# Optimization experiments

Measured on AMD Instinct MI355X. Metric: run time of the kernel, lower is better.

The kernel has to match this reference:

```python
import jax, jax.numpy as jnp
import numpy as np

B, S, T, D, V = 512, 128, 128, 512, 128  # batch, enc len, dec steps (=longest_smi), dim_model, output_size


def setup_inputs() -> dict:
    key = jax.random.key(0)
    ks = jax.random.split(key, 17)
    sc = 0.05
    return {
        "e_all": jax.random.normal(ks[0], (B, S, D), jnp.float32),
        "e_h": jax.random.normal(ks[1], (1, B, D), jnp.float32),
        "e_c": jax.random.normal(ks[2], (1, B, D), jnp.float32),
        "target": jax.random.randint(ks[3], (B, T), 0, T),
        # params (Linear weights stored [in, out], y = x @ W + b)
        "E": jax.random.normal(ks[4], (T, D), jnp.float32) * sc,        # Embedding(longest_smi, D)
        "Wa": jax.random.normal(ks[5], (D, D), jnp.float32) * sc,
        "ba": jnp.zeros((D,), jnp.float32),
        "Ua": jax.random.normal(ks[6], (D, D), jnp.float32) * sc,
        "bu": jnp.zeros((D,), jnp.float32),
        "Va": jax.random.normal(ks[7], (D, 1), jnp.float32) * sc,
        "bv": jnp.zeros((1,), jnp.float32),
        "W_ih": jax.random.normal(ks[8], (2 * D, 4 * D), jnp.float32) * sc,
        "b_ih": jnp.zeros((4 * D,), jnp.float32),
        "W_hh": jax.random.normal(ks[9], (D, 4 * D), jnp.float32) * sc,
        "b_hh": jnp.zeros((4 * D,), jnp.float32),
        "W_out": jax.random.normal(ks[10], (D, V), jnp.float32) * sc,
        "b_out": jnp.zeros((V,), jnp.float32),
    }


def reference(e_all, e_h, e_c, target, E, Wa, ba, Ua, bu, Va, bv,
              W_ih, b_ih, W_hh, b_hh, W_out, b_out):
    Bb = e_all.shape[0]
    # teacher forcing: step 0 input is token 0 (SOS), then target[:, :-1]
    idx = jnp.concatenate([jnp.zeros((Bb, 1), target.dtype), target[:, :-1]], axis=1)  # [B,T]
    emb_all = E[idx]                       # [B,T,D] (dropout is identity in eval)
    keys_proj = e_all @ Ua + bu            # Ua(keys), loop-invariant  [B,S,D]
    h0, c0 = e_h[0], e_c[0]                # [B,D]

    def step(carry, emb):
        h, c = carry
        q = (h + c) @ Wa + ba                                   # [B,D]  Wa(query)
        s = jnp.tanh(q[:, None, :] + keys_proj) @ Va + bv       # [B,S,1]
        w = jax.nn.softmax(s[..., 0], axis=-1)                  # [B,S]
        ctx = jnp.einsum('bs,bsd->bd', w, e_all)                # [B,D]
        x = jnp.concatenate([emb, ctx], axis=-1)                # [B,2D]
        g = x @ W_ih + b_ih + h @ W_hh + b_hh                   # [B,4D], torch gate order i,f,g,o
        i_, f_, g_, o_ = jnp.split(g, 4, axis=-1)
        c2 = jax.nn.sigmoid(f_) * c + jax.nn.sigmoid(i_) * jnp.tanh(g_)
        h2 = jax.nn.sigmoid(o_) * jnp.tanh(c2)
        out = h2 @ W_out + b_out                                # [B,V]
        return (h2, c2), (out, w)

    _, (outs, attns) = jax.lax.scan(step, (h0, c0), jnp.swapaxes(emb_all, 0, 1))
    outputs = jax.nn.log_softmax(jnp.swapaxes(outs, 0, 1), axis=-1)  # [B,T,V]
    cross_attn = jnp.swapaxes(attns, 0, 1)                           # [B,T,S]
    return outputs, cross_attn
```

## Files before the change

### kernel.cpp

```cpp
#include <hip/hip_runtime.h>

#define B_ 512
#define S_ 128
#define T_ 128
#define D_ 512
#define V_ 128
#define LDW 72

typedef __attribute__((ext_vector_type(8))) short s16x8;
typedef __attribute__((ext_vector_type(4))) short s16x4;
typedef __attribute__((ext_vector_type(4))) float f32x4;

__device__ __forceinline__ float b2f(unsigned short h) {
    union { unsigned int u; float f; } x; x.u = ((unsigned int)h) << 16; return x.f;
}
__device__ __forceinline__ unsigned short f2b(float f) {
    union { float f; unsigned int u; } x; x.f = f;
    unsigned int u = x.u; u += 0x7FFFu + ((u >> 16) & 1u);
    return (unsigned short)(u >> 16);
}
#if __has_builtin(__builtin_amdgcn_rcpf)
__device__ __forceinline__ float rcp_f(float x) { return __builtin_amdgcn_rcpf(x); }
#else
__device__ __forceinline__ float rcp_f(float x) { return 1.0f / x; }
#endif
__device__ __forceinline__ float sigm(float x) { return rcp_f(1.0f + __expf(-x)); }
__device__ __forceinline__ float tanh_fast(float x) {
    float e = __expf(2.0f * fabsf(x));
    float r = 1.0f - 2.0f * rcp_f(e + 1.0f);
    return copysignf(r, x);
}
__device__ __forceinline__ float tanh_pade(float x) {
    float t = x * x;
    float num = x * fmaf(t, 105.0f + t, 945.0f);
    float den = fmaf(t, fmaf(t, 15.0f, 420.0f), 945.0f);
    float r = num * rcp_f(den);
    return fminf(1.0f, fmaxf(-1.0f, r));
}

#if __has_builtin(__builtin_amdgcn_cvt_f32_fp8)
__device__ __forceinline__ f32x4 fp8x4_dec(unsigned w) {
    f32x4 r;
    r[0] = __builtin_amdgcn_cvt_f32_fp8(w, 0);
    r[1] = __builtin_amdgcn_cvt_f32_fp8(w, 1);
    r[2] = __builtin_amdgcn_cvt_f32_fp8(w, 2);
    r[3] = __builtin_amdgcn_cvt_f32_fp8(w, 3);
    return r;
}
#else
__device__ __forceinline__ float fp8_dec_sw(unsigned w, int j) {
    unsigned char v = (w >> (8 * j)) & 0xFF;
    unsigned s = v >> 7, e = (v >> 3) & 0xF, m = v & 7;
    float r = (e == 0) ? ldexpf((float)m, -9) : ldexpf((float)(8 + m), (int)e - 10);
    return s ? -r : r;
}
__device__ __forceinline__ f32x4 fp8x4_dec(unsigned w) {
    f32x4 r;
    r[0] = fp8_dec_sw(w, 0); r[1] = fp8_dec_sw(w, 1);
    r[2] = fp8_dec_sw(w, 2); r[3] = fp8_dec_sw(w, 3);
    return r;
}
#endif

#if __has_builtin(__builtin_amdgcn_cvt_pk_fp8_f32)
__device__ __forceinline__ unsigned pk_fp8(float a, float b, float c, float d) {
    int r = 0;
    r = __builtin_amdgcn_cvt_pk_fp8_f32(a, b, r, false);
    r = __builtin_amdgcn_cvt_pk_fp8_f32(c, d, r, true);
    return (unsigned)r;
}
#else
__device__ __forceinline__ unsigned char f32_to_fp8_sw(float x) {
    unsigned s = x < 0.f ? 0x80u : 0u; float a = fabsf(x);
    if (a != a) return (unsigned char)(s | 0x7F);
    if (a >= 448.f) return (unsigned char)(s | 0x7E);
    if (a < 0.001953125f) { int m = (int)rintf(a * 512.0f); return (unsigned char)(s | (m > 7 ? 0x08 : m)); }
    int e; float fr = frexpf(a, &e);
    int m = (int)rintf(fr * 16.0f - 8.0f);
    int ee = e - 1 + 7;
    if (m == 8) { m = 0; ee += 1; }
    if (ee <= 0) { int mm = (int)rintf(a * 512.f); return (unsigned char)(s | (mm > 7 ? 0x08 : mm)); }
    if (ee >= 16) return (unsigned char)(s | 0x7E);
    return (unsigned char)(s | (ee << 3) | m);
}
__device__ __forceinline__ unsigned pk_fp8(float a, float b, float c, float d) {
    return (unsigned)f32_to_fp8_sw(a) | ((unsigned)f32_to_fp8_sw(b) << 8)
         | ((unsigned)f32_to_fp8_sw(c) << 16) | ((unsigned)f32_to_fp8_sw(d) << 24);
}
#endif

struct P {
    const int* target;
    const float* E; const float* bv; const float* ba; const float* bout;
    const short* vab;
    const unsigned char* ea8; const unsigned char* kp8;
    const short* WaT; const short* WehT; const short* WctxT; const short* WoutT;
    const float* bcat;
    short* qbf; short* xeh; short* ctxb; short* gpA; short* gpB;
    short* hcbf; short* h2bf; float* cst;
    float* out_logits; float* out_attn;
};

struct AttnS { float scp[4][64]; float wbuf[S_]; float cpart[4][D_]; };
struct OutS  { short As[64][LDW]; short Bs[128][LDW]; };
struct PG2   { short As[128][LDW]; short Bs[64][LDW]; };
struct GateS { short As[64][LDW]; short Bs[64][LDW]; float gt[64][65]; };
union SharedC { OutS o; PG2 g; };

__device__ __forceinline__ void attn_phase(const P& p, AttnS& sh, int b, int step)
{
    const int t = threadIdx.x, lane = t & 63, wave = t >> 6;
    {
        const int sg = wave & 1, dh = wave >> 1;
        const int s = sg * 64 + lane;
        const unsigned char* kb = p.kp8 + (size_t)b * (S_ * D_);
        const short* qv = p.qbf + (size_t)b * D_;
        float acc = 0.f;
        #pragma unroll 4
        for (int i = 0; i < 16; ++i) {
            int g = dh * 16 + i;
            uint4 kw = *(const uint4*)(kb + ((size_t)g * 128 + s) * 16);
            const short* qg = qv + g * 16;
            const short* vg = p.vab + g * 16;
            s16x8 q0 = *(const s16x8*)(qg), q1 = *(const s16x8*)(qg + 8);
            s16x8 v0 = *(const s16x8*)(vg), v1 = *(const s16x8*)(vg + 8);
            f32x4 ka = fp8x4_dec(kw.x), kb4 = fp8x4_dec(kw.y);
            f32x4 kc = fp8x4_dec(kw.z), kd = fp8x4_dec(kw.w);
            #pragma unroll
            for (int j = 0; j < 4; ++j) {
                acc += tanh_pade(b2f((unsigned short)q0[j])     + ka[j])  * b2f((unsigned short)v0[j]);
                acc += tanh_pade(b2f((unsigned short)q0[4 + j]) + kb4[j]) * b2f((unsigned short)v0[4 + j]);
                acc += tanh_pade(b2f((unsigned short)q1[j])     + kc[j])  * b2f((unsigned short)v1[j]);
                acc += tanh_pade(b2f((unsigned short)q1[4 + j]) + kd[j])  * b2f((unsigned short)v1[4 + j]);
            }
        }
        sh.scp[wave][lane] = acc;
    }
    __syncthreads();
    if (wave == 0) {
        const float bvv = p.bv[0];
        float v0 = sh.scp[0][lane] + sh.scp[2][lane] + bvv;
        float v1 = sh.scp[1][lane] + sh.scp[3][lane] + bvv;
        float m = fmaxf(v0, v1);
        #pragma unroll
        for (int o = 32; o >= 1; o >>= 1) m = fmaxf(m, __shfl_xor(m, o));
        float e0 = __expf(v0 - m), e1 = __expf(v1 - m);
        float su = e0 + e1;
        #pragma unroll
        for (int o = 32; o >= 1; o >>= 1) su += __shfl_xor(su, o);
        float inv = rcp_f(su);
        float w0 = e0 * inv, w1 = e1 * inv;
        sh.wbuf[lane] = w0; sh.wbuf[lane + 64] = w1;
        float* ao = p.out_attn + ((size_t)b * T_ + step) * S_;
        ao[lane] = w0; ao[lane + 64] = w1;
    }
    __syncthreads();
    {
        const int d0 = lane * 8;
        f32x4 aA = {0.f,0.f,0.f,0.f}, aB = {0.f,0.f,0.f,0.f};
        const unsigned char* eb = p.ea8 + (size_t)b * S_ * D_ + d0;
        #pragma unroll 4
        for (int i = 0; i < 32; ++i) {
            int s = wave * 32 + i;
            float wv = sh.wbuf[s];
            uint2 ev = *(const uint2*)(eb + (size_t)s * D_);
            f32x4 ex = fp8x4_dec(ev.x), ey = fp8x4_dec(ev.y);
            #pragma unroll
            for (int j = 0; j < 4; ++j) aA[j] += wv * ex[j];
            #pragma unroll
            for (int j = 0; j < 4; ++j) aB[j] += wv * ey[j];
        }
        *(f32x4*)&sh.cpart[wave][d0]     = aA;
        *(f32x4*)&sh.cpart[wave][d0 + 4] = aB;
    }
    __syncthreads();
    {
        int dd = t * 2;
        float v0 = sh.cpart[0][dd]   + sh.cpart[1][dd]   + sh.cpart[2][dd]   + sh.cpart[3][dd];
        float v1 = sh.cpart[0][dd+1] + sh.cpart[1][dd+1] + sh.cpart[2][dd+1] + sh.cpart[3][dd+1];
        short2 o2; o2.x = (short)f2b(v0); o2.y = (short)f2b(v1);
        *(short2*)(p.ctxb + (size_t)b * D_ + dd) = o2;
    }
}

__device__ __forceinline__ void pgate_phase(const P& p, PG2& sh, int bid2, int koff,
                                            short* __restrict__ gpp, bool addb)
{
    const int t = threadIdx.x, lane = t & 63, wave = t >> 6;
    const int lrow = lane & 15, kq = lane >> 4;
    const int m0 = (bid2 >> 5) * 128, n0 = (bid2 & 31) * 64;
    f32x4 acc[2][4] = {};
    for (int k0 = 0; k0 < 512; k0 += 64) {
        s16x8 va[4], vb[2];
        #pragma unroll
        for (int r = 0; r < 4; ++r) {
            int idx = r * 256 + t, row = idx >> 3, seg = idx & 7;
            va[r] = *(const s16x8*)(p.xeh + (size_t)(m0 + row) * 1024 + koff + k0 + seg * 8);
        }
        #pragma unroll
        for (int r = 0; r < 2; ++r) {
            int idx = r * 256 + t, row = idx >> 3, seg = idx & 7;
            vb[r] = *(const s16x8*)(p.WehT + (size_t)(n0 + row) * 1024 + koff + k0 + seg * 8);
        }
        __syncthreads();
        #pragma unroll
        for (int r = 0; r < 4; ++r) {
            int idx = r * 256 + t, row = idx >> 3, seg = idx & 7;
            *(s16x8*)(&sh.As[row][seg * 8]) = va[r];
        }
        #pragma unroll
        for (int r = 0; r < 2; ++r) {
            int idx = r * 256 + t, row = idx >> 3, seg = idx & 7;
            *(s16x8*)(&sh.Bs[row][seg * 8]) = vb[r];
        }
        __syncthreads();
        #pragma unroll
        for (int kk = 0; kk < 64; kk += 32) {
            s16x8 af[2], bf[4];
            af[0] = *(const s16x8*)(&sh.As[wave * 32 + lrow][kk + kq * 8]);
            af[1] = *(const s16x8*)(&sh.As[wave * 32 + 16 + lrow][kk + kq * 8]);
            #pragma unroll
            for (int f = 0; f < 4; ++f)
                bf[f] = *(const s16x8*)(&sh.Bs[f * 16 + lrow][kk + kq * 8]);
            #pragma unroll
            for (int m2 = 0; m2 < 2; ++m2)
                #pragma unroll
                for (int n2 = 0; n2 < 4; ++n2)
                    acc[m2][n2] = __builtin_amdgcn_mfma_f32_16x16x32_bf16(af[m2], bf[n2], acc[m2][n2], 0, 0, 0);
        }
    }
    #pragma unroll
    for (int m2 = 0; m2 < 2; ++m2)
        #pragma unroll
        for (int n2 = 0; n2 < 4; ++n2) {
            int col = n0 + n2 * 16 + lrow;
            float bvv = addb ? p.bcat[col] : 0.0f;
            #pragma unroll
            for (int j = 0; j < 4; ++j) {
                int row = m0 + wave * 32 + m2 * 16 + kq * 4 + j;
                gpp[(size_t)row * 2048 + col] = (short)f2b(acc[m2][n2][j] + bvv);
            }
        }
}

__device__ __forceinline__ void fgate_phase(const P& p, GateS& sh, int bid, int step)
{
    const int t = threadIdx.x, lane = t & 63, wave = t >> 6;
    const int wr = wave >> 1, wc = wave & 1;
    const int lrow = lane & 15, kq = lane >> 4;
    const int srow = t >> 3, sseg = t & 7;
    const int m0 = (bid >> 5) * 64, n0 = (bid & 31) * 64;
    f32x4 acc[2][2] = {};
    for (int k0 = 0; k0 < 512; k0 += 64) {
        s16x8 va0 = *(const s16x8*)(p.ctxb + (size_t)(m0 + srow) * 512 + k0 + sseg * 8);
        s16x8 va1 = *(const s16x8*)(p.ctxb + (size_t)(m0 + srow + 32) * 512 + k0 + sseg * 8);
        s16x8 vb0 = *(const s16x8*)(p.WctxT + (size_t)(n0 + srow) * 512 + k0 + sseg * 8);
        s16x8 vb1 = *(const s16x8*)(p.WctxT + (size_t)(n0 + srow + 32) * 512 + k0 + sseg * 8);
        __syncthreads();
        *(s16x8*)(&sh.As[srow][sseg * 8]) = va0;
        *(s16x8*)(&sh.As[srow + 32][sseg * 8]) = va1;
        *(s16x8*)(&sh.Bs[srow][sseg * 8]) = vb0;
        *(s16x8*)(&sh.Bs[srow + 32][sseg * 8]) = vb1;
        __syncthreads();
        #pragma unroll
        for (int kk = 0; kk < 64; kk += 32) {
            s16x8 af0 = *(const s16x8*)(&sh.As[wr * 32 + lrow][kk + kq * 8]);
            s16x8 af1 = *(const s16x8*)(&sh.As[wr * 32 + 16 + lrow][kk + kq * 8]);
            s16x8 bf0 = *(const s16x8*)(&sh.Bs[wc * 32 + lrow][kk + kq * 8]);
            s16x8 bf1 = *(const s16x8*)(&sh.Bs[wc * 32 + 16 + lrow][kk + kq * 8]);
            acc[0][0] = __builtin_amdgcn_mfma_f32_16x16x32_bf16(af0, bf0, acc[0][0], 0, 0, 0);
            acc[0][1] = __builtin_amdgcn_mfma_f32_16x16x32_bf16(af0, bf1, acc[0][1], 0, 0, 0);
            acc[1][0] = __builtin_amdgcn_mfma_f32_16x16x32_bf16(af1, bf0, acc[1][0], 0, 0, 0);
            acc[1][1] = __builtin_amdgcn_mfma_f32_16x16x32_bf16(af1, bf1, acc[1][1], 0, 0, 0);
        }
    }
    #pragma unroll
    for (int m2 = 0; m2 < 2; ++m2)
        #pragma unroll
        for (int n2 = 0; n2 < 2; ++n2) {
            int cl = wc * 32 + n2 * 16 + lrow;
            #pragma unroll
            for (int j = 0; j < 4; ++j) {
                int rl = wr * 32 + m2 * 16 + kq * 4 + j;
                size_t gidx = (size_t)(m0 + rl) * 2048 + n0 + cl;
                sh.gt[rl][cl] = acc[m2][n2][j]
                              + b2f((unsigned short)p.gpA[gidx])
                              + b2f((unsigned short)p.gpB[gidx]);
            }
        }
    __syncthreads();
    const int rl4 = t >> 4, dl = t & 15;
    #pragma unroll
    for (int pass = 0; pass < 4; ++pass) {
        int row = pass * 16 + rl4;
        int b = m0 + row;
        int d = (n0 >> 2) + dl;
        float gi = sh.gt[row][dl * 4 + 0];
        float gf = sh.gt[row][dl * 4 + 1];
        float gg = sh.gt[row][dl * 4 + 2];
        float go = sh.gt[row][dl * 4 + 3];
        float cv = p.cst[(size_t)b * D_ + d];
        float c2 = sigm(gf) * cv + sigm(gi) * tanh_fast(gg);
        float h2 = sigm(go) * tanh_fast(c2);
        p.cst[(size_t)b * D_ + d] = c2;
        p.hcbf[(size_t)b * D_ + d] = (short)f2b(h2 + c2);
        p.h2bf[(size_t)b * D_ + d] = (short)f2b(h2);
        p.xeh[(size_t)b * 1024 + 512 + d] = (short)f2b(h2);
        int tok = p.target[b * T_ + step];
        p.xeh[(size_t)b * 1024 + d] = (short)f2b(p.E[(size_t)tok * D_ + d]);
    }
}

__device__ __forceinline__ void q_phase(const P& p, OutS& sh, int bid)
{
    const int t = threadIdx.x, lane = t & 63, wave = t >> 6;
    const int lrow = lane & 15, kq = lane >> 4;
    const int srow = t >> 3, sseg = t & 7;
    const int m0 = (bid >> 4) * 64, n0 = (bid & 15) * 32;
    f32x4 acc0 = {}, acc1 = {};
    for (int k0 = 0; k0 < 512; k0 += 64) {
        s16x8 va0 = *(const s16x8*)(p.hcbf + (size_t)(m0 + srow) * 512 + k0 + sseg * 8);
        s16x8 va1 = *(const s16x8*)(p.hcbf + (size_t)(m0 + srow + 32) * 512 + k0 + sseg * 8);
        int brow = n0 + (srow & 31);
        s16x8 vb0 = *(const s16x8*)(p.WaT + (size_t)brow * 512 + k0 + sseg * 8);
        __syncthreads();
        *(s16x8*)(&sh.As[srow][sseg * 8]) = va0;
        *(s16x8*)(&sh.As[srow + 32][sseg * 8]) = va1;
        if (srow < 32) *(s16x8*)(&sh.Bs[srow][sseg * 8]) = vb0;
        __syncthreads();
        #pragma unroll
        for (int kk = 0; kk < 64; kk += 32) {
            s16x8 af  = *(const s16x8*)(&sh.As[wave * 16 + lrow][kk + kq * 8]);
            s16x8 bf0 = *(const s16x8*)(&sh.Bs[lrow][kk + kq * 8]);
            s16x8 bf1 = *(const s16x8*)(&sh.Bs[16 + lrow][kk + kq * 8]);
            acc0 = __builtin_amdgcn_mfma_f32_16x16x32_bf16(af, bf0, acc0, 0, 0, 0);
            acc1 = __builtin_amdgcn_mfma_f32_16x16x32_bf16(af, bf1, acc1, 0, 0, 0);
        }
    }
    #pragma unroll
    for (int n2 = 0; n2 < 2; ++n2) {
        int col = n0 + n2 * 16 + lrow;
        float bvv = p.ba[col];
        f32x4 av = n2 ? acc1 : acc0;
        #pragma unroll
        for (int j = 0; j < 4; ++j) {
            int row = m0 + wave * 16 + kq * 4 + j;
            p.qbf[(size_t)row * 512 + col] = (short)f2b(av[j] + bvv);
        }
    }
}

__device__ __forceinline__ void out_phase(const P& p, OutS& sh, int obid, int step)
{
    const int t = threadIdx.x, lane = t & 63, wave = t >> 6;
    const int lrow = lane & 15, kq = lane >> 4;
    const int srow = t >> 3, sseg = t & 7;
    const int m0 = obid * 64;
    f32x4 acc[8] = {};
    for (int k0 = 0; k0 < 512; k0 += 64) {
        s16x8 va0 = *(const s16x8*)(p.h2bf + (size_t)(m0 + srow) * 512 + k0 + sseg * 8);
        s16x8 va1 = *(const s16x8*)(p.h2bf + (size_t)(m0 + srow + 32) * 512 + k0 + sseg * 8);
        s16x8 vb[4];
        #pragma unroll
        for (int p4 = 0; p4 < 4; ++p4)
            vb[p4] = *(const s16x8*)(p.WoutT + (size_t)(srow + p4 * 32) * 512 + k0 + sseg * 8);
        __syncthreads();
        *(s16x8*)(&sh.As[srow][sseg * 8]) = va0;
        *(s16x8*)(&sh.As[srow + 32][sseg * 8]) = va1;
        #pragma unroll
        for (int p4 = 0; p4 < 4; ++p4) *(s16x8*)(&sh.Bs[srow + p4 * 32][sseg * 8]) = vb[p4];
        __syncthreads();
        #pragma unroll
        for (int kk = 0; kk < 64; kk += 32) {
            s16x8 a = *(const s16x8*)(&sh.As[wave * 16 + lrow][kk + kq * 8]);
            #pragma unroll
            for (int f = 0; f < 8; ++f) {
                s16x8 b = *(const s16x8*)(&sh.Bs[f * 16 + lrow][kk + kq * 8]);
                acc[f] = __builtin_amdgcn_mfma_f32_16x16x32_bf16(a, b, acc[f], 0, 0, 0);
            }
        }
    }
    float colb[8];
    #pragma unroll
    for (int f = 0; f < 8; ++f) colb[f] = p.bout[f * 16 + lrow];
    #pragma unroll
    for (int j = 0; j < 4; ++j) {
        float v[8]; float mx = -1e30f;
        #pragma unroll
        for (int f = 0; f < 8; ++f) { v[f] = acc[f][j] + colb[f]; mx = fmaxf(mx, v[f]); }
        #pragma unroll
        for (int o = 1; o < 16; o <<= 1) mx = fmaxf(mx, __shfl_xor(mx, o));
        float sum = 0.f;
        #pragma unroll
        for (int f = 0; f < 8; ++f) sum += __expf(v[f] - mx);
        #pragma unroll
        for (int o = 1; o < 16; o <<= 1) sum += __shfl_xor(sum, o);
        float lse = mx + __logf(sum);
        int row = m0 + wave * 16 + kq * 4 + j;
        float* orow = p.out_logits + ((size_t)row * T_ + step) * V_;
        #pragma unroll
        for (int f = 0; f < 8; ++f) orow[f * 16 + lrow] = v[f] - lse;
    }
}

__global__ __launch_bounds__(256, 2) void kA(P p, int step) {
    __shared__ AttnS sh;
    attn_phase(p, sh, blockIdx.x, step);
}
__global__ __launch_bounds__(256, 2) void kB(P p, int step) {
    __shared__ GateS sh;
    fgate_phase(p, sh, blockIdx.x, step);
}
template<bool INIT>
__global__ __launch_bounds__(256, 2) void kC(P p, int step) {
    __shared__ SharedC sh;
    const int bid = blockIdx.x;
    if (bid < 128)       q_phase(p, sh.o, bid);
    else if (bid < 256)  pgate_phase(p, sh.g, bid - 128, 0,   p.gpA, true);
    else if (bid < 384)  pgate_phase(p, sh.g, bid - 256, 512, p.gpB, false);
    else if (!INIT)      out_phase(p, sh.o, bid - 384, step);
}

__global__ __launch_bounds__(256)
void gemm64(const short* __restrict__ A, const short* __restrict__ Bt,
            const float* __restrict__ bias, short* __restrict__ Cp,
            int M, int N, int K)
{
    __shared__ __align__(16) short As[64][LDW];
    __shared__ __align__(16) short Bs[64][LDW];
    const int t = threadIdx.x;
    const int lane = t & 63, wave = t >> 6;
    const int wr = wave >> 1, wc = wave & 1;
    const int lrow = lane & 15, kq = lane >> 4;
    const int m0 = blockIdx.y * 64, n0 = blockIdx.x * 64;
    const int srow = t >> 3, sseg = t & 7;
    f32x4 acc[2][2] = {};
    for (int k0 = 0; k0 < K; k0 += 64) {
        s16x8 va0 = *(const s16x8*)(A + (size_t)(m0 + srow) * K + k0 + sseg * 8);
        s16x8 va1 = *(const s16x8*)(A + (size_t)(m0 + srow + 32) * K + k0 + sseg * 8);
        s16x8 vb0 = *(const s16x8*)(Bt + (size_t)(n0 + srow) * K + k0 + sseg * 8);
        s16x8 vb1 = *(const s16x8*)(Bt + (size_t)(n0 + srow + 32) * K + k0 + sseg * 8);
        __syncthreads();
        *(s16x8*)(&As[srow][sseg * 8]) = va0;
        *(s16x8*)(&As[srow + 32][sseg * 8]) = va1;
        *(s16x8*)(&Bs[srow][sseg * 8]) = vb0;
        *(s16x8*)(&Bs[srow + 32][sseg * 8]) = vb1;
        __syncthreads();
        for (int kk = 0; kk < 64; kk += 32) {
            s16x8 af[2], bf[2];
            af[0] = *(const s16x8*)(&As[wr * 32 + lrow][kk + kq * 8]);
            af[1] = *(const s16x8*)(&As[wr * 32 + 16 + lrow][kk + kq * 8]);
            bf[0] = *(const s16x8*)(&Bs[wc * 32 + lrow][kk + kq * 8]);
            bf[1] = *(const s16x8*)(&Bs[wc * 32 + 16 + lrow][kk + kq * 8]);
            for (int m2 = 0; m2 < 2; ++m2)
                for (int n2 = 0; n2 < 2; ++n2)
                    acc[m2][n2] = __builtin_amdgcn_mfma_f32_16x16x32_bf16(af[m2], bf[n2], acc[m2][n2], 0, 0, 0);
        }
    }
    for (int m2 = 0; m2 < 2; ++m2)
        for (int n2 = 0; n2 < 2; ++n2) {
            int col = n0 + wc * 32 + n2 * 16 + lrow;
            float bvv = bias ? bias[col] : 0.0f;
            for (int j = 0; j < 4; ++j) {
                int row = m0 + wr * 32 + m2 * 16 + kq * 4 + j;
                Cp[(size_t)row * N + col] = (short)f2b(acc[m2][n2][j] + bvv);
            }
        }
}

__global__ __launch_bounds__(256)
void transpose_kp8(const short* __restrict__ in, unsigned char* __restrict__ out)
{
    const int b = blockIdx.x, t = threadIdx.x;
    const size_t ibase = (size_t)b * (S_ * D_);
    for (int k = t; k < 32 * S_; k += 256) {
        int g = k >> 7, s = k & 127;
        const short* src = in + ibase + (size_t)s * D_ + g * 16;
        unsigned w[4];
        #pragma unroll
        for (int q4 = 0; q4 < 4; ++q4) {
            w[q4] = pk_fp8(b2f((unsigned short)src[q4 * 4 + 0]), b2f((unsigned short)src[q4 * 4 + 1]),
                           b2f((unsigned short)src[q4 * 4 + 2]), b2f((unsigned short)src[q4 * 4 + 3]));
        }
        uint4 o; o.x = w[0]; o.y = w[1]; o.z = w[2]; o.w = w[3];
        *(uint4*)(out + ibase + ((size_t)g * S_ + s) * 16) = o;
    }
}

__global__ __launch_bounds__(256)
void cast_fp8_v4(const float* __restrict__ in, unsigned char* __restrict__ out, int n4)
{
    int i = blockIdx.x * 256 + threadIdx.x;
    int stride = gridDim.x * 256;
    for (; i < n4; i += stride) {
        f32x4 v = ((const f32x4*)in)[i];
        ((unsigned*)out)[i] = pk_fp8(v[0], v[1], v[2], v[3]);
    }
}

__global__ __launch_bounds__(256)
void init_state(const float* __restrict__ e_h, const float* __restrict__ e_c,
                float* __restrict__ c, short* __restrict__ hcbf,
                short* __restrict__ xeh, const float* __restrict__ E)
{
    int gid = blockIdx.x * 256 + threadIdx.x;
    int b = gid >> 9, d = gid & 511;
    float h0 = e_h[gid], c0 = e_c[gid];
    c[gid] = c0;
    hcbf[gid] = (short)f2b(h0 + c0);
    xeh[(size_t)b * 1024 + 512 + d] = (short)f2b(h0);
    xeh[(size_t)b * 1024 + d] = (short)f2b(E[d]);
}

__global__ __launch_bounds__(256)
void transpose_cast(const float* __restrict__ in, short* __restrict__ out,
                    int N, int ostride, int koff, int gate_perm)
{
    __shared__ float tile[64][65];
    int t = threadIdx.x;
    int n0 = blockIdx.x * 64, k0 = blockIdx.y * 64;
    int cc = t & 63, r4 = t >> 6;
    for (int i = 0; i < 16; ++i) {
        int r = i * 4 + r4;
        tile[r][cc] = in[(size_t)(k0 + r) * N + n0 + cc];
    }
    __syncthreads();
    for (int i = 0; i < 16; ++i) {
        int nr = i * 4 + r4;
        int ng = n0 + nr;
        int np = gate_perm ? ((ng & 511) * 4 + (ng >> 9)) : ng;
        out[(size_t)np * ostride + koff + k0 + cc] = (short)f2b(tile[cc][nr]);
    }
}

__global__ __launch_bounds__(256)
void cast_bf16_v4(const float* __restrict__ in, short* __restrict__ out, int n4)
{
    int i = blockIdx.x * 256 + threadIdx.x;
    int stride = gridDim.x * 256;
    for (; i < n4; i += stride) {
        f32x4 v = ((const f32x4*)in)[i];
        s16x4 o;
        for (int j = 0; j < 4; ++j) o[j] = (short)f2b(v[j]);
        ((s16x4*)out)[i] = o;
    }
}

__global__ __launch_bounds__(256)
void make_bcat(const float* __restrict__ b_ih, const float* __restrict__ b_hh, float* __restrict__ bcat)
{
    int i = blockIdx.x * 256 + threadIdx.x;
    if (i < 2048) {
        int np = (i & 511) * 4 + (i >> 9);
        bcat[np] = b_ih[i] + b_hh[i];
    }
}

extern "C" void kernel_launch(void* const* d_in, const int* in_sizes, int n_in,
                              void* d_out, int out_size, void* d_ws, size_t ws_size,
                              hipStream_t stream)
{
    const float* e_all  = (const float*)d_in[0];
    const float* e_h    = (const float*)d_in[1];
    const float* e_c    = (const float*)d_in[2];
    const int*   target = (const int*)d_in[3];
    const float* E      = (const float*)d_in[4];
    const float* Wa     = (const float*)d_in[5];
    const float* ba     = (const float*)d_in[6];
    const float* Ua     = (const float*)d_in[7];
    const float* bu     = (const float*)d_in[8];
    const float* Va     = (const float*)d_in[9];
    const float* bv     = (const float*)d_in[10];
    const float* W_ih   = (const float*)d_in[11];
    const float* b_ih   = (const float*)d_in[12];
    const float* W_hh   = (const float*)d_in[13];
    const float* b_hh   = (const float*)d_in[14];
    const float* W_out  = (const float*)d_in[15];
    const float* b_out  = (const float*)d_in[16];

    char* ws = (char*)d_ws;
    size_t off = 0;
    auto alloc = [&](size_t bytes) { void* p = ws + off; off += (bytes + 255) & ~255ull; return p; };
    short* ealb  = (short*)alloc((size_t)B_ * S_ * D_ * 2);
    short* kpb   = (short*)alloc((size_t)B_ * S_ * D_ * 2);
    unsigned char* kp8 = (unsigned char*)alloc((size_t)B_ * S_ * D_);
    unsigned char* ea8 = (unsigned char*)alloc((size_t)B_ * S_ * D_);
    short* WaT   = (short*)alloc((size_t)D_ * D_ * 2);
    short* UaT   = (short*)alloc((size_t)D_ * D_ * 2);
    short* WehT  = (short*)alloc((size_t)2048 * 1024 * 2);
    short* WctxT = (short*)alloc((size_t)2048 * 512 * 2);
    short* WoutT = (short*)alloc((size_t)V_ * D_ * 2);
    float* bcat  = (float*)alloc(2048 * 4);
    short* qbf   = (short*)alloc((size_t)B_ * D_ * 2);
    short* vab   = (short*)alloc((size_t)D_ * 2);
    short* xeh   = (short*)alloc((size_t)B_ * 1024 * 2);
    short* ctxb  = (short*)alloc((size_t)B_ * D_ * 2);
    short* gpA   = (short*)alloc((size_t)B_ * 2048 * 2);
    short* gpB   = (short*)alloc((size_t)B_ * 2048 * 2);
    short* hcbf  = (short*)alloc((size_t)B_ * D_ * 2);
    short* h2bf  = (short*)alloc((size_t)B_ * D_ * 2);
    float* cst   = (float*)alloc((size_t)B_ * D_ * 4);
    if (off > ws_size) return;

    float* out_logits = (float*)d_out;
    float* out_attn   = (float*)d_out + (size_t)B_ * T_ * V_;

    cast_bf16_v4<<<4096, 256, 0, stream>>>(e_all, ealb, B_ * S_ * D_ / 4);
    cast_fp8_v4<<<4096, 256, 0, stream>>>(e_all, ea8, B_ * S_ * D_ / 4);
    cast_bf16_v4<<<1,    256, 0, stream>>>(Va, vab, D_ / 4);
    transpose_cast<<<dim3(8, 8),  256, 0, stream>>>(Wa,  WaT,  512,  512, 0, 0);
    transpose_cast<<<dim3(8, 8),  256, 0, stream>>>(Ua,  UaT,  512,  512, 0, 0);
    transpose_cast<<<dim3(32, 8), 256, 0, stream>>>(W_ih,              WehT,  2048, 1024, 0,   1);
    transpose_cast<<<dim3(32, 8), 256, 0, stream>>>(W_ih + 512 * 2048, WctxT, 2048, 512,  0,   1);
    transpose_cast<<<dim3(32, 8), 256, 0, stream>>>(W_hh,              WehT,  2048, 1024, 512, 1);
    transpose_cast<<<dim3(2, 8),  256, 0, stream>>>(W_out, WoutT, 128, 512, 0, 0);
    make_bcat<<<8, 256, 0, stream>>>(b_ih, b_hh, bcat);
    gemm64<<<dim3(8, 1024), 256, 0, stream>>>(ealb, UaT, bu, kpb, B_ * S_, 512, 512);
    transpose_kp8<<<512, 256, 0, stream>>>(kpb, kp8);
    init_state<<<1024, 256, 0, stream>>>(e_h, e_c, cst, hcbf, xeh, E);

    P pp;
    pp.target = target; pp.E = E; pp.bv = bv; pp.ba = ba; pp.bout = b_out;
    pp.vab = vab;
    pp.ea8 = ea8; pp.kp8 = kp8; pp.WaT = WaT; pp.WehT = WehT; pp.WctxT = WctxT; pp.WoutT = WoutT;
    pp.bcat = bcat; pp.qbf = qbf; pp.xeh = xeh; pp.ctxb = ctxb; pp.gpA = gpA; pp.gpB = gpB;
    pp.hcbf = hcbf; pp.h2bf = h2bf; pp.cst = cst;
    pp.out_logits = out_logits; pp.out_attn = out_attn;

    kC<true><<<384, 256, 0, stream>>>(pp, 0);

    for (int t = 0; t < T_; ++t) {
        kA<<<512, 256, 0, stream>>>(pp, t);
        kB<<<256, 256, 0, stream>>>(pp, t);
        kC<false><<<392, 256, 0, stream>>>(pp, t);
    }
    (void)n_in; (void)in_sizes; (void)out_size;
}
```

Before: 6.259 ms.

## Fuse query projection into attention and merge per-step kernels into two launches

Removes the separate q=(h+c)@Wa GEMM by computing it inside the attention block, with each block handling two batch rows. The attention kernel now also runs the full-K emb/h gate pre-GEMM (the two half-K partials are merged into one buffer) and the previous step's output projection, so each time step needs two launches instead of three. The aim is to cut launch and inter-kernel sync overhead and the extra global round trips for q and the partial gates. In exchange, the q projection runs on scalar FMAs that re-read Wa for every pair of rows, and attention blocks do more serial work each.

```diff
diff --git a/kernel.cpp b/kernel.cpp
--- a/kernel.cpp
+++ b/kernel.cpp
@@ -91,36 +91,67 @@
 
 struct P {
     const int* target;
-    const float* E; const float* bv; const float* ba; const float* bout;
+    const float* E; const float* bv; const float* ba; const float* bout; const float* bcat;
     const short* vab;
     const unsigned char* ea8; const unsigned char* kp8;
-    const short* WaT; const short* WehT; const short* WctxT; const short* WoutT;
-    const float* bcat;
-    short* qbf; short* xeh; short* ctxb; short* gpA; short* gpB;
-    short* hcbf; short* h2bf; float* cst;
+    const short* Wab; const short* WehT; const short* WctxT; const short* WoutT;
+    short* ctxb; short* gp;
+    float* cst; short* hcbf; short* h2bf; short* xeh;
     float* out_logits; float* out_attn;
 };
 
-struct AttnS { float scp[4][64]; float wbuf[S_]; float cpart[4][D_]; };
+struct Attn2S {
+    float hcl[2][512];
+    float part[4][512];
+    short qbls[2][512];
+    float scp[4][64];
+    float wbuf[2][128];
+};
+struct PG2   { short As[128][LDW]; short Bs[64][LDW]; };
 struct OutS  { short As[64][LDW]; short Bs[128][LDW]; };
-struct PG2   { short As[128][LDW]; short Bs[64][LDW]; };
 struct GateS { short As[64][LDW]; short Bs[64][LDW]; float gt[64][65]; };
-union SharedC { OutS o; PG2 g; };
-
-__device__ __forceinline__ void attn_phase(const P& p, AttnS& sh, int b, int step)
+union SharedD1 { Attn2S a; PG2 pg; OutS o; };
+
+__device__ __forceinline__ void attn2_phase(const P& p, Attn2S& sh, int pairIdx, int step)
 {
     const int t = threadIdx.x, lane = t & 63, wave = t >> 6;
+    const int r = wave >> 1;
+    const int b0 = pairIdx * 2;
+    for (int i = t; i < 1024; i += 256) {
+        int rr = i >> 9, d = i & 511;
+        sh.hcl[rr][d] = b2f((unsigned short)p.hcbf[(size_t)(b0 + rr) * 512 + d]);
+    }
+    __syncthreads();
     {
-        const int sg = wave & 1, dh = wave >> 1;
+        const int kh = wave & 1;
+        const short* wb = p.Wab + (size_t)(kh * 256) * 512 + lane * 8;
+        float qa[8] = {};
+        #pragma unroll 4
+        for (int k = 0; k < 256; ++k) {
+            s16x8 wv = *(const s16x8*)(wb + (size_t)k * 512);
+            float h = sh.hcl[r][kh * 256 + k];
+            #pragma unroll
+            for (int j = 0; j < 8; ++j) qa[j] += h * b2f((unsigned short)wv[j]);
+        }
+        #pragma unroll
+        for (int j = 0; j < 8; ++j) sh.part[wave][lane * 8 + j] = qa[j];
+    }
+    __syncthreads();
+    for (int i = t; i < 1024; i += 256) {
+        int rr = i >> 9, c = i & 511;
+        float qv = sh.part[rr * 2][c] + sh.part[rr * 2 + 1][c] + p.ba[c];
+        sh.qbls[rr][c] = (short)f2b(qv);
+    }
+    __syncthreads();
+    {
+        const int sg = wave & 1;
         const int s = sg * 64 + lane;
-        const unsigned char* kb = p.kp8 + (size_t)b * (S_ * D_);
-        const short* qv = p.qbf + (size_t)b * D_;
+        const unsigned char* kb = p.kp8 + (size_t)(b0 + r) * (S_ * D_);
         float acc = 0.f;
-        #pragma unroll 4
-        for (int i = 0; i < 16; ++i) {
-            int g = dh * 16 + i;
+        #pragma unroll 2
+        for (int g = 0; g < 32; ++g) {
             uint4 kw = *(const uint4*)(kb + ((size_t)g * 128 + s) * 16);
-            const short* qg = qv + g * 16;
+            const short* qg = &sh.qbls[r][g * 16];
             const short* vg = p.vab + g * 16;
             s16x8 q0 = *(const s16x8*)(qg), q1 = *(const s16x8*)(qg + 8);
             s16x8 v0 = *(const s16x8*)(vg), v1 = *(const s16x8*)(vg + 8);
@@ -137,10 +168,10 @@
         sh.scp[wave][lane] = acc;
     }
     __syncthreads();
-    if (wave == 0) {
+    if ((wave & 1) == 0) {
         const float bvv = p.bv[0];
-        float v0 = sh.scp[0][lane] + sh.scp[2][lane] + bvv;
-        float v1 = sh.scp[1][lane] + sh.scp[3][lane] + bvv;
+        float v0 = sh.scp[wave][lane] + bvv;
+        float v1 = sh.scp[wave + 1][lane] + bvv;
         float m = fmaxf(v0, v1);
         #pragma unroll
         for (int o = 32; o >= 1; o >>= 1) m = fmaxf(m, __shfl_xor(m, o));
@@ -150,19 +181,20 @@
         for (int o = 32; o >= 1; o >>= 1) su += __shfl_xor(su, o);
         float inv = rcp_f(su);
         float w0 = e0 * inv, w1 = e1 * inv;
-        sh.wbuf[lane] = w0; sh.wbuf[lane + 64] = w1;
-        float* ao = p.out_attn + ((size_t)b * T_ + step) * S_;
+        sh.wbuf[r][lane] = w0; sh.wbuf[r][lane + 64] = w1;
+        float* ao = p.out_attn + ((size_t)(b0 + r) * T_ + step) * S_;
         ao[lane] = w0; ao[lane + 64] = w1;
     }
     __syncthreads();
     {
+        const int sg = wave & 1;
         const int d0 = lane * 8;
         f32x4 aA = {0.f,0.f,0.f,0.f}, aB = {0.f,0.f,0.f,0.f};
-        const unsigned char* eb = p.ea8 + (size_t)b * S_ * D_ + d0;
+        const unsigned char* eb = p.ea8 + (size_t)(b0 + r) * S_ * D_ + d0;
         #pragma unroll 4
-        for (int i = 0; i < 32; ++i) {
-            int s = wave * 32 + i;
-            float wv = sh.wbuf[s];
+        for (int i = 0; i < 64; ++i) {
+            int s = sg * 64 + i;
+            float wv = sh.wbuf[r][s];
             uint2 ev = *(const uint2*)(eb + (size_t)s * D_);
             f32x4 ex = fp8x4_dec(ev.x), ey = fp8x4_dec(ev.y);
             #pragma unroll
@@ -170,37 +202,39 @@
             #pragma unroll
             for (int j = 0; j < 4; ++j) aB[j] += wv * ey[j];
         }
-        *(f32x4*)&sh.cpart[wave][d0]     = aA;
-        *(f32x4*)&sh.cpart[wave][d0 + 4] = aB;
+        *(f32x4*)&sh.part[wave][d0]     = aA;
+        *(f32x4*)&sh.part[wave][d0 + 4] = aB;
     }
     __syncthreads();
     {
         int dd = t * 2;
-        float v0 = sh.cpart[0][dd]   + sh.cpart[1][dd]   + sh.cpart[2][dd]   + sh.cpart[3][dd];
-        float v1 = sh.cpart[0][dd+1] + sh.cpart[1][dd+1] + sh.cpart[2][dd+1] + sh.cpart[3][dd+1];
-        short2 o2; o2.x = (short)f2b(v0); o2.y = (short)f2b(v1);
-        *(short2*)(p.ctxb + (size_t)b * D_ + dd) = o2;
-    }
-}
-
-__device__ __forceinline__ void pgate_phase(const P& p, PG2& sh, int bid2, int koff,
-                                            short* __restrict__ gpp, bool addb)
+        #pragma unroll
+        for (int rr = 0; rr < 2; ++rr) {
+            float v0 = sh.part[rr * 2][dd]     + sh.part[rr * 2 + 1][dd];
+            float v1 = sh.part[rr * 2][dd + 1] + sh.part[rr * 2 + 1][dd + 1];
+            short2 o2; o2.x = (short)f2b(v0); o2.y = (short)f2b(v1);
+            *(short2*)(p.ctxb + (size_t)(b0 + rr) * D_ + dd) = o2;
+        }
+    }
+}
+
+__device__ __forceinline__ void pgate_full(const P& p, PG2& sh, int bid2)
 {
     const int t = threadIdx.x, lane = t & 63, wave = t >> 6;
     const int lrow = lane & 15, kq = lane >> 4;
     const int m0 = (bid2 >> 5) * 128, n0 = (bid2 & 31) * 64;
     f32x4 acc[2][4] = {};
-    for (int k0 = 0; k0 < 512; k0 += 64) {
+    for (int k0 = 0; k0 < 1024; k0 += 64) {
         s16x8 va[4], vb[2];
         #pragma unroll
         for (int r = 0; r < 4; ++r) {
             int idx = r * 256 + t, row = idx >> 3, seg = idx & 7;
-            va[r] = *(const s16x8*)(p.xeh + (size_t)(m0 + row) * 1024 + koff + k0 + seg * 8);
+            va[r] = *(const s16x8*)(p.xeh + (size_t)(m0 + row) * 1024 + k0 + seg * 8);
         }
         #pragma unroll
         for (int r = 0; r < 2; ++r) {
             int idx = r * 256 + t, row = idx >> 3, seg = idx & 7;
-            vb[r] = *(const s16x8*)(p.WehT + (size_t)(n0 + row) * 1024 + koff + k0 + seg * 8);
+            vb[r] = *(const s16x8*)(p.WehT + (size_t)(n0 + row) * 1024 + k0 + seg * 8);
         }
         __syncthreads();
         #pragma unroll
@@ -234,21 +268,76 @@
         #pragma unroll
         for (int n2 = 0; n2 < 4; ++n2) {
             int col = n0 + n2 * 16 + lrow;
-            float bvv = addb ? p.bcat[col] : 0.0f;
+            float bvv = p.bcat[col];
             #pragma unroll
             for (int j = 0; j < 4; ++j) {
                 int row = m0 + wave * 32 + m2 * 16 + kq * 4 + j;
-                gpp[(size_t)row * 2048 + col] = (short)f2b(acc[m2][n2][j] + bvv);
+                p.gp[(size_t)row * 2048 + col] = (short)f2b(acc[m2][n2][j] + bvv);
             }
         }
 }
 
-__device__ __forceinline__ void fgate_phase(const P& p, GateS& sh, int bid, int step)
-{
+__device__ __forceinline__ void out_phase(const P& p, OutS& sh, int obid, int step)
+{
+    const int t = threadIdx.x, lane = t & 63, wave = t >> 6;
+    const int lrow = lane & 15, kq = lane >> 4;
+    const int srow = t >> 3, sseg = t & 7;
+    const int m0 = obid * 64;
+    f32x4 acc[8] = {};
+    for (int k0 = 0; k0 < 512; k0 += 64) {
+        s16x8 va0 = *(const s16x8*)(p.h2bf + (size_t)(m0 + srow) * 512 + k0 + sseg * 8);
+        s16x8 va1 = *(const s16x8*)(p.h2bf + (size_t)(m0 + srow + 32) * 512 + k0 + sseg * 8);
+        s16x8 vb[4];
+        #pragma unroll
+        for (int p4 = 0; p4 < 4; ++p4)
+            vb[p4] = *(const s16x8*)(p.WoutT + (size_t)(srow + p4 * 32) * 512 + k0 + sseg * 8);
+        __syncthreads();
+        *(s16x8*)(&sh.As[srow][sseg * 8]) = va0;
+        *(s16x8*)(&sh.As[srow + 32][sseg * 8]) = va1;
+        #pragma unroll
+        for (int p4 = 0; p4 < 4; ++p4) *(s16x8*)(&sh.Bs[srow + p4 * 32][sseg * 8]) = vb[p4];
+        __syncthreads();
+        #pragma unroll
+        for (int kk = 0; kk < 64; kk += 32) {
+            s16x8 a = *(const s16x8*)(&sh.As[wave * 16 + lrow][kk + kq * 8]);
+            #pragma unroll
+            for (int f = 0; f < 8; ++f) {
+                s16x8 b = *(const s16x8*)(&sh.Bs[f * 16 + lrow][kk + kq * 8]);
+                acc[f] = __builtin_amdgcn_mfma_f32_16x16x32_bf16(a, b, acc[f], 0, 0, 0);
+            }
+        }
+    }
+    float colb[8];
+    #pragma unroll
+    for (int f = 0; f < 8; ++f) colb[f] = p.bout[f * 16 + lrow];
+    #pragma unroll
+    for (int j = 0; j < 4; ++j) {
+        float v[8]; float mx = -1e30f;
+        #pragma unroll
+        for (int f = 0; f < 8; ++f) { v[f] = acc[f][j] + colb[f]; mx = fmaxf(mx, v[f]); }
+        #pragma unroll
+        for (int o = 1; o < 16; o <<= 1) mx = fmaxf(mx, __shfl_xor(mx, o));
+        float sum = 0.f;
+        #pragma unroll
+        for (int f = 0; f < 8; ++f) sum += __expf(v[f] - mx);
+        #pragma unroll
+        for (int o = 1; o < 16; o <<= 1) sum += __shfl_xor(sum, o);
+        float lse = mx + __logf(sum);
+        int row = m0 + wave * 16 + kq * 4 + j;
+        float* orow = p.out_logits + ((size_t)row * T_ + step) * V_;
+        #pragma unroll
+        for (int f = 0; f < 8; ++f) orow[f * 16 + lrow] = v[f] - lse;
+    }
+}
+
+__global__ __launch_bounds__(256, 2) void kB(P p, int step)
+{
+    __shared__ GateS sh;
     const int t = threadIdx.x, lane = t & 63, wave = t >> 6;
     const int wr = wave >> 1, wc = wave & 1;
     const int lrow = lane & 15, kq = lane >> 4;
     const int srow = t >> 3, sseg = t & 7;
+    const int bid = blockIdx.x;
     const int m0 = (bid >> 5) * 64, n0 = (bid & 31) * 64;
     f32x4 acc[2][2] = {};
     for (int k0 = 0; k0 < 512; k0 += 64) {
@@ -282,143 +371,54 @@
             #pragma unroll
             for (int j = 0; j < 4; ++j) {
                 int rl = wr * 32 + m2 * 16 + kq * 4 + j;
-                size_t gidx = (size_t)(m0 + rl) * 2048 + n0 + cl;
                 sh.gt[rl][cl] = acc[m2][n2][j]
-                              + b2f((unsigned short)p.gpA[gidx])
-                              + b2f((unsigned short)p.gpB[gidx]);
+                              + b2f((unsigned short)p.gp[(size_t)(m0 + rl) * 2048 + n0 + cl]);
             }
         }
     __syncthreads();
-    const int rl4 = t >> 4, dl = t & 15;
+    const int dp = t & 7, rr = t >> 3;
     #pragma unroll
-    for (int pass = 0; pass < 4; ++pass) {
-        int row = pass * 16 + rl4;
+    for (int pass = 0; pass < 2; ++pass) {
+        int row = pass * 32 + rr;
         int b = m0 + row;
-        int d = (n0 >> 2) + dl;
-        float gi = sh.gt[row][dl * 4 + 0];
-        float gf = sh.gt[row][dl * 4 + 1];
-        float gg = sh.gt[row][dl * 4 + 2];
-        float go = sh.gt[row][dl * 4 + 3];
-        float cv = p.cst[(size_t)b * D_ + d];
-        float c2 = sigm(gf) * cv + sigm(gi) * tanh_fast(gg);
-        float h2 = sigm(go) * tanh_fast(c2);
-        p.cst[(size_t)b * D_ + d] = c2;
-        p.hcbf[(size_t)b * D_ + d] = (short)f2b(h2 + c2);
-        p.h2bf[(size_t)b * D_ + d] = (short)f2b(h2);
-        p.xeh[(size_t)b * 1024 + 512 + d] = (short)f2b(h2);
+        int dl0 = dp * 2;
+        float gi0 = sh.gt[row][dl0 * 4 + 0], gf0 = sh.gt[row][dl0 * 4 + 1];
+        float gg0 = sh.gt[row][dl0 * 4 + 2], go0 = sh.gt[row][dl0 * 4 + 3];
+        float gi1 = sh.gt[row][dl0 * 4 + 4], gf1 = sh.gt[row][dl0 * 4 + 5];
+        float gg1 = sh.gt[row][dl0 * 4 + 6], go1 = sh.gt[row][dl0 * 4 + 7];
+        int d = (n0 >> 2) + dl0;
+        float2 cv = *(const float2*)(p.cst + (size_t)b * 512 + d);
+        float c20 = sigm(gf0) * cv.x + sigm(gi0) * tanh_fast(gg0);
+        float h20 = sigm(go0) * tanh_fast(c20);
+        float c21 = sigm(gf1) * cv.y + sigm(gi1) * tanh_fast(gg1);
+        float h21 = sigm(go1) * tanh_fast(c21);
+        float2 cw; cw.x = c20; cw.y = c21;
+        *(float2*)(p.cst + (size_t)b * 512 + d) = cw;
+        unsigned hcp = (unsigned)f2b(h20 + c20) | ((unsigned)f2b(h21 + c21) << 16);
+        unsigned h2p = (unsigned)f2b(h20) | ((unsigned)f2b(h21) << 16);
+        *(unsigned*)(p.hcbf + (size_t)b * 512 + d) = hcp;
+        *(unsigned*)(p.h2bf + (size_t)b * 512 + d) = h2p;
+        *(unsigned*)(p.xeh + (size_t)b * 1024 + 512 + d) = h2p;
         int tok = p.target[b * T_ + step];
-        p.xeh[(size_t)b * 1024 + d] = (short)f2b(p.E[(size_t)tok * D_ + d]);
-    }
-}
-
-__device__ __forceinline__ void q_phase(const P& p, OutS& sh, int bid)
-{
-    const int t = threadIdx.x, lane = t & 63, wave = t >> 6;
-    const int lrow = lane & 15, kq = lane >> 4;
-    const int srow = t >> 3, sseg = t & 7;
-    const int m0 = (bid >> 4) * 64, n0 = (bid & 15) * 32;
-    f32x4 acc0 = {}, acc1 = {};
-    for (int k0 = 0; k0 < 512; k0 += 64) {
-        s16x8 va0 = *(const s16x8*)(p.hcbf + (size_t)(m0 + srow) * 512 + k0 + sseg * 8);
-        s16x8 va1 = *(const s16x8*)(p.hcbf + (size_t)(m0 + srow + 32) * 512 + k0 + sseg * 8);
-        int brow = n0 + (srow & 31);
-        s16x8 vb0 = *(const s16x8*)(p.WaT + (size_t)brow * 512 + k0 + sseg * 8);
-        __syncthreads();
-        *(s16x8*)(&sh.As[srow][sseg * 8]) = va0;
-        *(s16x8*)(&sh.As[srow + 32][sseg * 8]) = va1;
-        if (srow < 32) *(s16x8*)(&sh.Bs[srow][sseg * 8]) = vb0;
-        __syncthreads();
-        #pragma unroll
-        for (int kk = 0; kk < 64; kk += 32) {
-            s16x8 af  = *(const s16x8*)(&sh.As[wave * 16 + lrow][kk + kq * 8]);
-            s16x8 bf0 = *(const s16x8*)(&sh.Bs[lrow][kk + kq * 8]);
-            s16x8 bf1 = *(const s16x8*)(&sh.Bs[16 + lrow][kk + kq * 8]);
-            acc0 = __builtin_amdgcn_mfma_f32_16x16x32_bf16(af, bf0, acc0, 0, 0, 0);
-            acc1 = __builtin_amdgcn_mfma_f32_16x16x32_bf16(af, bf1, acc1, 0, 0, 0);
-        }
-    }
-    #pragma unroll
-    for (int n2 = 0; n2 < 2; ++n2) {
-        int col = n0 + n2 * 16 + lrow;
-        float bvv = p.ba[col];
-        f32x4 av = n2 ? acc1 : acc0;
-        #pragma unroll
-        for (int j = 0; j < 4; ++j) {
-            int row = m0 + wave * 16 + kq * 4 + j;
-            p.qbf[(size_t)row * 512 + col] = (short)f2b(av[j] + bvv);
-        }
-    }
-}
-
-__device__ __forceinline__ void out_phase(const P& p, OutS& sh, int obid, int step)
-{
-    const int t = threadIdx.x, lane = t & 63, wave = t >> 6;
-    const int lrow = lane & 15, kq = lane >> 4;
-    const int srow = t >> 3, sseg = t & 7;
-    const int m0 = obid * 64;
-    f32x4 acc[8] = {};
-    for (int k0 = 0; k0 < 512; k0 += 64) {
-        s16x8 va0 = *(const s16x8*)(p.h2bf + (size_t)(m0 + srow) * 512 + k0 + sseg * 8);
-        s16x8 va1 = *(const s16x8*)(p.h2bf + (size_t)(m0 + srow + 32) * 512 + k0 + sseg * 8);
-        s16x8 vb[4];
-        #pragma unroll
-        for (int p4 = 0; p4 < 4; ++p4)
-            vb[p4] = *(const s16x8*)(p.WoutT + (size_t)(srow + p4 * 32) * 512 + k0 + sseg * 8);
-        __syncthreads();
-        *(s16x8*)(&sh.As[srow][sseg * 8]) = va0;
-        *(s16x8*)(&sh.As[srow + 32][sseg * 8]) = va1;
-        #pragma unroll
-        for (int p4 = 0; p4 < 4; ++p4) *(s16x8*)(&sh.Bs[srow + p4 * 32][sseg * 8]) = vb[p4];
-        __syncthreads();
-        #pragma unroll
-        for (int kk = 0; kk < 64; kk += 32) {
-            s16x8 a = *(const s16x8*)(&sh.As[wave * 16 + lrow][kk + kq * 8]);
-            #pragma unroll
-            for (int f = 0; f < 8; ++f) {
-                s16x8 b = *(const s16x8*)(&sh.Bs[f * 16 + lrow][kk + kq * 8]);
-                acc[f] = __builtin_amdgcn_mfma_f32_16x16x32_bf16(a, b, acc[f], 0, 0, 0);
-            }
-        }
-    }
-    float colb[8];
-    #pragma unroll
-    for (int f = 0; f < 8; ++f) colb[f] = p.bout[f * 16 + lrow];
-    #pragma unroll
-    for (int j = 0; j < 4; ++j) {
-        float v[8]; float mx = -1e30f;
-        #pragma unroll
-        for (int f = 0; f < 8; ++f) { v[f] = acc[f][j] + colb[f]; mx = fmaxf(mx, v[f]); }
-        #pragma unroll
-        for (int o = 1; o < 16; o <<= 1) mx = fmaxf(mx, __shfl_xor(mx, o));
-        float sum = 0.f;
-        #pragma unroll
-        for (int f = 0; f < 8; ++f) sum += __expf(v[f] - mx);
-        #pragma unroll
-        for (int o = 1; o < 16; o <<= 1) sum += __shfl_xor(sum, o);
-        float lse = mx + __logf(sum);
-        int row = m0 + wave * 16 + kq * 4 + j;
-        float* orow = p.out_logits + ((size_t)row * T_ + step) * V_;
-        #pragma unroll
-        for (int f = 0; f < 8; ++f) orow[f * 16 + lrow] = v[f] - lse;
-    }
-}
-
-__global__ __launch_bounds__(256, 2) void kA(P p, int step) {
-    __shared__ AttnS sh;
-    attn_phase(p, sh, blockIdx.x, step);
-}
-__global__ __launch_bounds__(256, 2) void kB(P p, int step) {
-    __shared__ GateS sh;
-    fgate_phase(p, sh, blockIdx.x, step);
-}
-template<bool INIT>
-__global__ __launch_bounds__(256, 2) void kC(P p, int step) {
-    __shared__ SharedC sh;
+        unsigned ep = (unsigned)f2b(p.E[(size_t)tok * 512 + d])
+                    | ((unsigned)f2b(p.E[(size_t)tok * 512 + d + 1]) << 16);
+        *(unsigned*)(p.xeh + (size_t)b * 1024 + d) = ep;
+    }
+}
+
+__global__ __launch_bounds__(256, 2) void kD1(P p, int step)
+{
+    __shared__ SharedD1 sh;
     const int bid = blockIdx.x;
-    if (bid < 128)       q_phase(p, sh.o, bid);
-    else if (bid < 256)  pgate_phase(p, sh.g, bid - 128, 0,   p.gpA, true);
-    else if (bid < 384)  pgate_phase(p, sh.g, bid - 256, 512, p.gpB, false);
-    else if (!INIT)      out_phase(p, sh.o, bid - 384, step);
+    if (bid < 256)       attn2_phase(p, sh.a, bid, step);
+    else if (bid < 384)  pgate_full(p, sh.pg, bid - 256);
+    else if (step > 0)   out_phase(p, sh.o, bid - 384, step - 1);
+}
+
+__global__ __launch_bounds__(256, 2) void kOutLast(P p, int step)
+{
+    __shared__ OutS sh;
+    out_phase(p, sh, blockIdx.x, step);
 }
 
 __global__ __launch_bounds__(256)
@@ -585,18 +585,16 @@
     short* kpb   = (short*)alloc((size_t)B_ * S_ * D_ * 2);
     unsigned char* kp8 = (unsigned char*)alloc((size_t)B_ * S_ * D_);
     unsigned char* ea8 = (unsigned char*)alloc((size_t)B_ * S_ * D_);
-    short* WaT   = (short*)alloc((size_t)D_ * D_ * 2);
+    short* Wab   = (short*)alloc((size_t)D_ * D_ * 2);
     short* UaT   = (short*)alloc((size_t)D_ * D_ * 2);
     short* WehT  = (short*)alloc((size_t)2048 * 1024 * 2);
     short* WctxT = (short*)alloc((size_t)2048 * 512 * 2);
     short* WoutT = (short*)alloc((size_t)V_ * D_ * 2);
     float* bcat  = (float*)alloc(2048 * 4);
-    short* qbf   = (short*)alloc((size_t)B_ * D_ * 2);
     short* vab   = (short*)alloc((size_t)D_ * 2);
     short* xeh   = (short*)alloc((size_t)B_ * 1024 * 2);
     short* ctxb  = (short*)alloc((size_t)B_ * D_ * 2);
-    short* gpA   = (short*)alloc((size_t)B_ * 2048 * 2);
-    short* gpB   = (short*)alloc((size_t)B_ * 2048 * 2);
+    short* gp    = (short*)alloc((size_t)B_ * 2048 * 2);
     short* hcbf  = (short*)alloc((size_t)B_ * D_ * 2);
     short* h2bf  = (short*)alloc((size_t)B_ * D_ * 2);
     float* cst   = (float*)alloc((size_t)B_ * D_ * 4);
@@ -608,7 +606,7 @@
     cast_bf16_v4<<<4096, 256, 0, stream>>>(e_all, ealb, B_ * S_ * D_ / 4);
     cast_fp8_v4<<<4096, 256, 0, stream>>>(e_all, ea8, B_ * S_ * D_ / 4);
     cast_bf16_v4<<<1,    256, 0, stream>>>(Va, vab, D_ / 4);
-    transpose_cast<<<dim3(8, 8),  256, 0, stream>>>(Wa,  WaT,  512,  512, 0, 0);
+    cast_bf16_v4<<<256,  256, 0, stream>>>(Wa, Wab, D_ * D_ / 4);
     transpose_cast<<<dim3(8, 8),  256, 0, stream>>>(Ua,  UaT,  512,  512, 0, 0);
     transpose_cast<<<dim3(32, 8), 256, 0, stream>>>(W_ih,              WehT,  2048, 1024, 0,   1);
     transpose_cast<<<dim3(32, 8), 256, 0, stream>>>(W_ih + 512 * 2048, WctxT, 2048, 512,  0,   1);
@@ -620,19 +618,17 @@
     init_state<<<1024, 256, 0, stream>>>(e_h, e_c, cst, hcbf, xeh, E);
 
     P pp;
-    pp.target = target; pp.E = E; pp.bv = bv; pp.ba = ba; pp.bout = b_out;
-    pp.vab = vab;
-    pp.ea8 = ea8; pp.kp8 = kp8; pp.WaT = WaT; pp.WehT = WehT; pp.WctxT = WctxT; pp.WoutT = WoutT;
-    pp.bcat = bcat; pp.qbf = qbf; pp.xeh = xeh; pp.ctxb = ctxb; pp.gpA = gpA; pp.gpB = gpB;
-    pp.hcbf = hcbf; pp.h2bf = h2bf; pp.cst = cst;
+    pp.target = target; pp.E = E; pp.bv = bv; pp.ba = ba; pp.bout = b_out; pp.bcat = bcat;
+    pp.vab = vab; pp.ea8 = ea8; pp.kp8 = kp8;
+    pp.Wab = Wab; pp.WehT = WehT; pp.WctxT = WctxT; pp.WoutT = WoutT;
+    pp.ctxb = ctxb; pp.gp = gp;
+    pp.cst = cst; pp.hcbf = hcbf; pp.h2bf = h2bf; pp.xeh = xeh;
     pp.out_logits = out_logits; pp.out_attn = out_attn;
 
-    kC<true><<<384, 256, 0, stream>>>(pp, 0);
-
     for (int t = 0; t < T_; ++t) {
-        kA<<<512, 256, 0, stream>>>(pp, t);
+        kD1<<<392, 256, 0, stream>>>(pp, t);
         kB<<<256, 256, 0, stream>>>(pp, t);
-        kC<false><<<392, 256, 0, stream>>>(pp, t);
-    }
+    }
+    kOutLast<<<8, 256, 0, stream>>>(pp, T_ - 1);
     (void)n_in; (void)in_sizes; (void)out_size;
 }
```

Result: slower. 7.824 ms (+25.0%).
